# Performance work log

Measured on AMD Instinct MI355X. Metric: run time of the kernel, lower is better.

## Reference

```python
import jax, jax.numpy as jnp
import numpy as np


def dct_matrices(N):
    # torch_dct-style unnormalized DCT-II (norm=None): X_k = 2 * sum_n x_n cos(pi*(2n+1)k/(2N))
    n = jnp.arange(N, dtype=jnp.float32)
    ang = jnp.pi * (2.0 * n[None, :] + 1.0) * n[:, None] / (2.0 * N)  # [k, n]
    D = 2.0 * jnp.cos(ang)                                            # forward DCT matrix [k, n]
    w = jnp.where(n == 0, 0.5, 1.0)                                   # half-weight on DC term
    M = (jnp.cos(ang).T * w[None, :]) / (2.0 * N)                     # inverse DCT matrix [n, k]
    return D, M


def setup_inputs() -> dict:
    key = jax.random.key(0)
    k1, k2, k3 = jax.random.split(key, 3)
    B, c_in, c_out, H, W, kh, kw = 8, 64, 128, 128, 128, 5, 5
    K = float(np.sqrt(1.0 / (c_in * kh * kw)))
    x = jax.random.normal(k1, (B, c_in, H, W), dtype=jnp.float32)
    weight = (2.0 * jax.random.uniform(k2, (c_out, c_in, kh, kw), dtype=jnp.float32) - 1.0) * K
    bias = (2.0 * jax.random.uniform(k3, (c_out,), dtype=jnp.float32) - 1.0) * K
    return {"x": x, "weight": weight, "bias": bias}


def reference(x, weight, bias):
    B, c_in, H, W = x.shape
    c_out, _, kh, kw = weight.shape
    D, M = dct_matrices(H)

    # DCT-II along H axis of input
    xd = jnp.einsum('kh,bchw->bckw', D, x)            # (B, c_in, H, W)
    xf = jnp.fft.rfft(xd, axis=-1)                    # (B, c_in, H, Wf) complex

    # Pad kernel along H to full size, DCT along H, rFFT along W with n=W
    wpad = jnp.pad(weight, ((0, 0), (0, 0), (0, H - kh), (0, 0)))
    wd = jnp.einsum('kh,oihw->oikw', D, wpad)         # (c_out, c_in, H, kw)
    wf = jnp.fft.rfft(wd, n=W, axis=-1)               # (c_out, c_in, H, Wf) complex

    # Broadcast complex multiply + reduce over c_in (fused via einsum)
    hf = jnp.einsum('bchw,ochw->bohw', xf, wf)        # (B, c_out, H, Wf)
    h = jnp.fft.irfft(hf, n=W, axis=-1)               # (B, c_out, H, W)

    # Inverse DCT along H, add bias, stride slice (stride = 1)
    h = jnp.einsum('nk,bokw->bonw', M, h) + bias[None, :, None, None]
    return h[:, :, ::1, ::1]
```

## Files before the change

### kernel.cpp

```cpp
#include <hip/hip_runtime.h>


using half8v = __attribute__((ext_vector_type(8))) _Float16;
using half4v = __attribute__((ext_vector_type(4))) _Float16;
using f32x4  = __attribute__((ext_vector_type(4))) float;

#define PI_F 3.14159265358979323846f

__device__ __forceinline__ int sw_off(int n, int k, int K, int mask) {
    int c = k >> 3;
    return n * K + (((c ^ (n & mask)) << 3) | (k & 7));
}

__global__ void k_dm(_Float16* __restrict__ D, _Float16* __restrict__ M) {
    int k = blockIdx.x;
    int h = threadIdx.x;
    float ang = PI_F * (float)((2 * h + 1) * k) * (1.0f / 256.0f);
    float c = cosf(ang);
    D[k * 128 + h] = (_Float16)(2.0f * c);
    float wk = (k == 0) ? 0.5f : 1.0f;
    M[h * 128 + k] = (_Float16)(c * wk * (1.0f / 256.0f));
}

__global__ __launch_bounds__(256) void k_wd(const float* __restrict__ w, _Float16* __restrict__ WD) {
    __shared__ float lw[1600];
    __shared__ float lcos[320];
    int co = blockIdx.x >> 1, k0 = (blockIdx.x & 1) << 6;
    int tid = threadIdx.x;

    for (int e = tid; e < 1600; e += 256) lw[e] = w[co * 1600 + e];
    for (int e = tid; e < 320; e += 256) {
        int kl = e / 5, i = e - kl * 5;
        lcos[e] = 2.0f * cosf(PI_F * (float)((2 * i + 1) * (k0 + kl)) * (1.0f / 256.0f));
    }
    __syncthreads();

    for (int e = tid; e < 20480; e += 256) {
        int kk = e & 31, rest = e >> 5;
        int s = rest % 10, kl = rest / 10;
        int j = s >> 1, ci = ((s & 1) << 5) + kk;
        const float* wp = &lw[ci * 25 + j];
        const float* cp = &lcos[kl * 5];
        float acc = 0.f;
#pragma unroll
        for (int i = 0; i < 5; ++i) acc += cp[i] * wp[i * 5];
        WD[(((long)(k0 + kl) * 10 + s) * 128 + co) * 32 + kk] = (_Float16)acc;
    }
}

__device__ __forceinline__ void gemm128_gA(const _Float16* __restrict__ gA,
                                           const _Float16* lB,
                                           f32x4 acc[4][4], int tid) {
    int lane = tid & 63, ln = lane & 15, q = lane >> 4;
    int wave = tid >> 6, wm = wave >> 1, wn = wave & 1;
#pragma unroll
    for (int s = 0; s < 4; ++s) {
        half8v af[4], bf[4];
#pragma unroll
        for (int mt = 0; mt < 4; ++mt) {
            int m = wm * 64 + mt * 16 + ln;
            af[mt] = *(const half8v*)(&gA[m * 128 + (s * 4 + q) * 8]);
        }
#pragma unroll
        for (int nt = 0; nt < 4; ++nt) {
            int n = wn * 64 + nt * 16 + ln;
            bf[nt] = *(const half8v*)(&lB[n * 128 + (((s * 4 + q) ^ (n & 15)) << 3)]);
        }
#pragma unroll
        for (int mt = 0; mt < 4; ++mt)
#pragma unroll
            for (int nt = 0; nt < 4; ++nt)
                acc[mt][nt] = __builtin_amdgcn_mfma_f32_16x16x32_f16(af[mt], bf[nt], acc[mt][nt], 0, 0, 0);
    }
}

__device__ __forceinline__ void stage_transB(const _Float16* __restrict__ src, int row_stride,
                                             _Float16* l, int K, int mask, int nblocks, int tid) {
    for (int blk = tid; blk < nblocks; blk += 256) {
        int kb = blk >> 4, wb = blk & 15;
        int k0 = kb * 4, w0 = wb * 8;
        half8v r0 = *(const half8v*)(&src[(k0 + 0) * row_stride + w0]);
        half8v r1 = *(const half8v*)(&src[(k0 + 1) * row_stride + w0]);
        half8v r2 = *(const half8v*)(&src[(k0 + 2) * row_stride + w0]);
        half8v r3 = *(const half8v*)(&src[(k0 + 3) * row_stride + w0]);
#pragma unroll
        for (int dw = 0; dw < 8; ++dw) {
            int n = w0 + dw;
            half4v p = {r0[dw], r1[dw], r2[dw], r3[dw]};
            *(half4v*)(&l[sw_off(n, k0, K, mask)]) = p;
        }
    }
}

__global__ __launch_bounds__(256) void k_dctH(const float* __restrict__ x,
                                              const _Float16* __restrict__ Dg,
                                              _Float16* __restrict__ xd) {
    __shared__ _Float16 lB[128 * 128];
    int b = blockIdx.x >> 6, ci = blockIdx.x & 63;
    int tid = threadIdx.x;

    const float* xs = x + (long)(b * 64 + ci) * 16384;
#pragma unroll
    for (int rep = 0; rep < 2; ++rep) {
        int blk = tid + rep * 256;
        int hb = blk >> 4, wb = blk & 15;
        int h0 = hb * 4, w0 = wb * 8;
        f32x4 f[4][2];
#pragma unroll
        for (int dh = 0; dh < 4; ++dh) {
            f[dh][0] = *(const f32x4*)(&xs[(h0 + dh) * 128 + w0]);
            f[dh][1] = *(const f32x4*)(&xs[(h0 + dh) * 128 + w0 + 4]);
        }
#pragma unroll
        for (int dw = 0; dw < 8; ++dw) {
            int n = w0 + dw;
            half4v p = {(_Float16)f[0][dw >> 2][dw & 3], (_Float16)f[1][dw >> 2][dw & 3],
                        (_Float16)f[2][dw >> 2][dw & 3], (_Float16)f[3][dw >> 2][dw & 3]};
            *(half4v*)(&lB[sw_off(n, h0, 128, 15)]) = p;
        }
    }
    __syncthreads();

    f32x4 acc[4][4] = {};
    gemm128_gA(Dg, lB, acc, tid);

    int lane = tid & 63, ln = lane & 15, q = lane >> 4;
    int wave = tid >> 6, wm = wave >> 1, wn = wave & 1;
#pragma unroll
    for (int mt = 0; mt < 4; ++mt)
#pragma unroll
        for (int nt = 0; nt < 4; ++nt)
#pragma unroll
            for (int r = 0; r < 4; ++r) {
                int kk = wm * 64 + mt * 16 + q * 4 + r;
                int wcol = wn * 64 + nt * 16 + ln;
                xd[((long)(kk * 8 + b) * 64 + ci) * 128 + wcol] = (_Float16)acc[mt][nt][r];
            }
}

__global__ __launch_bounds__(256) void k_conv(const _Float16* __restrict__ xd,
                                              const _Float16* __restrict__ WD,
                                              _Float16* __restrict__ y2) {
    __shared__ _Float16 lX[128 * 64];
    int bid = blockIdx.x;
    int k = bid & 127, b = bid >> 7;
    int tid = threadIdx.x;

    const _Float16* xs = xd + (long)(k * 8 + b) * 8192;
    stage_transB(xs, 128, lX, 64, 7, 256, tid);
    __syncthreads();

    int lane = tid & 63, ln = lane & 15, q = lane >> 4;
    int wave = tid >> 6, wm = wave >> 1, wn = wave & 1;
    f32x4 acc[4][4] = {};

    const _Float16* wkb = WD + (long)k * 40960;

    for (int s = 0; s < 10; ++s) {
        int j = s >> 1;
        int cb = (s & 1) << 2;
        const _Float16* wt = wkb + s * 4096;
        half8v af[4], bf[4];
#pragma unroll
        for (int mt = 0; mt < 4; ++mt) {
            int m = wm * 64 + mt * 16 + ln;
            af[mt] = *(const half8v*)(&wt[m * 32 + q * 8]);
        }
#pragma unroll
        for (int nt = 0; nt < 4; ++nt) {
            int wcol = wn * 64 + nt * 16 + ln;
            int n = (wcol - j) & 127;
            bf[nt] = *(const half8v*)(&lX[n * 64 + (((cb + q) ^ (n & 7)) << 3)]);
        }
#pragma unroll
        for (int mt = 0; mt < 4; ++mt)
#pragma unroll
            for (int nt = 0; nt < 4; ++nt)
                acc[mt][nt] = __builtin_amdgcn_mfma_f32_16x16x32_f16(af[mt], bf[nt], acc[mt][nt], 0, 0, 0);
    }

    _Float16* yb = y2 + (long)(b * 128 + k) * 16384;
#pragma unroll
    for (int mt = 0; mt < 4; ++mt)
#pragma unroll
        for (int nt = 0; nt < 4; ++nt)
#pragma unroll
            for (int r = 0; r < 4; ++r) {
                int co = wm * 64 + mt * 16 + q * 4 + r;
                int wcol = wn * 64 + nt * 16 + ln;
                yb[co * 128 + wcol] = (_Float16)acc[mt][nt][r];
            }
}

__global__ __launch_bounds__(256) void k_idct(const _Float16* __restrict__ y2,
                                              const _Float16* __restrict__ Mg,
                                              const float* __restrict__ bias,
                                              float* __restrict__ out) {
    __shared__ _Float16 lB[128 * 128];
    int b = blockIdx.x >> 7, co = blockIdx.x & 127;
    int tid = threadIdx.x;

    const _Float16* src = y2 + (long)b * 2097152 + co * 128;
    stage_transB(src, 16384, lB, 128, 15, 512, tid);
    __syncthreads();

    f32x4 acc[4][4] = {};
    gemm128_gA(Mg, lB, acc, tid);

    float bv = bias[co];
    float* ob = out + ((long)(b * 128 + co)) * 16384;
    int lane = tid & 63, ln = lane & 15, q = lane >> 4;
    int wave = tid >> 6, wm = wave >> 1, wn = wave & 1;
#pragma unroll
    for (int mt = 0; mt < 4; ++mt)
#pragma unroll
        for (int nt = 0; nt < 4; ++nt)
#pragma unroll
            for (int r = 0; r < 4; ++r) {
                int h = wm * 64 + mt * 16 + q * 4 + r;
                int wcol = wn * 64 + nt * 16 + ln;
                ob[h * 128 + wcol] = acc[mt][nt][r] + bv;
            }
}

extern "C" void kernel_launch(void* const* d_in, const int* in_sizes, int n_in,
                              void* d_out, int out_size, void* d_ws, size_t ws_size,
                              hipStream_t stream) {
    const float* x    = (const float*)d_in[0];
    const float* w    = (const float*)d_in[1];
    const float* bias = (const float*)d_in[2];
    float* out = (float*)d_out;

    char* ws = (char*)d_ws;
    _Float16* D  = (_Float16*)(ws);
    _Float16* M  = (_Float16*)(ws + 32768);
    _Float16* WD = (_Float16*)(ws + 65536);
    _Float16* xd = (_Float16*)(ws + 65536 + 10485760);
    _Float16* y2 = (_Float16*)(ws + 65536 + 10485760 + 16777216);

    k_dm  <<<dim3(128),  dim3(128), 0, stream>>>(D, M);
    k_wd  <<<dim3(256),  dim3(256), 0, stream>>>(w, WD);
    k_dctH<<<dim3(512),  dim3(256), 0, stream>>>(x, D, xd);
    k_conv<<<dim3(1024), dim3(256), 0, stream>>>(xd, WD, y2);
    k_idct<<<dim3(1024), dim3(256), 0, stream>>>(y2, M, bias, out);
}
```

Measured before the change: 149.1 us.

## Double-buffer conv weights via async LDS loads, merge prep kernels, relayout y2

Result: faster. 144.6 us (-3.0%).

```diff
diff --git a/kernel.cpp b/kernel.cpp
--- a/kernel.cpp
+++ b/kernel.cpp
@@ -12,17 +12,15 @@
     return n * K + (((c ^ (n & mask)) << 3) | (k & 7));
 }
 
-__global__ void k_dm(_Float16* __restrict__ D, _Float16* __restrict__ M) {
-    int k = blockIdx.x;
-    int h = threadIdx.x;
-    float ang = PI_F * (float)((2 * h + 1) * k) * (1.0f / 256.0f);
-    float c = cosf(ang);
-    D[k * 128 + h] = (_Float16)(2.0f * c);
-    float wk = (k == 0) ? 0.5f : 1.0f;
-    M[h * 128 + k] = (_Float16)(c * wk * (1.0f / 256.0f));
-}
-
-__global__ __launch_bounds__(256) void k_wd(const float* __restrict__ w, _Float16* __restrict__ WD) {
+__device__ __forceinline__ void gload16(const _Float16* g, _Float16* l) {
+    __builtin_amdgcn_global_load_lds((const __attribute__((address_space(1))) void*)g,
+                                     (__attribute__((address_space(3))) void*)l, 16, 0, 0);
+}
+
+__global__ __launch_bounds__(256) void k_prep(const float* __restrict__ w,
+                                              _Float16* __restrict__ WD,
+                                              _Float16* __restrict__ D,
+                                              _Float16* __restrict__ M) {
     __shared__ float lw[1600];
     __shared__ float lcos[320];
     int co = blockIdx.x >> 1, k0 = (blockIdx.x & 1) << 6;
@@ -32,6 +30,15 @@
     for (int e = tid; e < 320; e += 256) {
         int kl = e / 5, i = e - kl * 5;
         lcos[e] = 2.0f * cosf(PI_F * (float)((2 * i + 1) * (k0 + kl)) * (1.0f / 256.0f));
+    }
+    if (tid < 64) {
+        int g = blockIdx.x * 64 + tid;
+        int k = g >> 7, h = g & 127;
+        float ang = PI_F * (float)((2 * h + 1) * k) * (1.0f / 256.0f);
+        float c = cosf(ang);
+        D[k * 128 + h] = (_Float16)(2.0f * c);
+        float wk = (k == 0) ? 0.5f : 1.0f;
+        M[h * 128 + k] = (_Float16)(c * wk * (1.0f / 256.0f));
     }
     __syncthreads();
 
@@ -142,24 +149,38 @@
                                               const _Float16* __restrict__ WD,
                                               _Float16* __restrict__ y2) {
     __shared__ _Float16 lX[128 * 64];
+    __shared__ _Float16 lW[2 * 4096];
     int bid = blockIdx.x;
     int k = bid & 127, b = bid >> 7;
     int tid = threadIdx.x;
+    int lane = tid & 63, wave = tid >> 6;
 
     const _Float16* xs = xd + (long)(k * 8 + b) * 8192;
     stage_transB(xs, 128, lX, 64, 7, 256, tid);
-    __syncthreads();
-
-    int lane = tid & 63, ln = lane & 15, q = lane >> 4;
-    int wave = tid >> 6, wm = wave >> 1, wn = wave & 1;
+
+    const _Float16* wkb = WD + (long)k * 40960;
+    {
+        int eo = wave * 512 + lane * 8;
+        gload16(&wkb[eo],            &lW[wave * 512]);
+        gload16(&wkb[2048 + eo],     &lW[2048 + wave * 512]);
+        gload16(&wkb[4096 + eo],     &lW[4096 + wave * 512]);
+        gload16(&wkb[6144 + eo],     &lW[4096 + 2048 + wave * 512]);
+    }
+    __syncthreads();
+
+    int ln = lane & 15, q = lane >> 4;
+    int wm = wave >> 1, wn = wave & 1;
     f32x4 acc[4][4] = {};
 
-    const _Float16* wkb = WD + (long)k * 40960;
-
     for (int s = 0; s < 10; ++s) {
+        if (s == 9) asm volatile("s_waitcnt vmcnt(0)" ::: "memory");
+        else        asm volatile("s_waitcnt vmcnt(2)" ::: "memory");
+        __builtin_amdgcn_s_barrier();
+        asm volatile("" ::: "memory");
+
+        const _Float16* wt = &lW[(s & 1) * 4096];
         int j = s >> 1;
         int cb = (s & 1) << 2;
-        const _Float16* wt = wkb + s * 4096;
         half8v af[4], bf[4];
 #pragma unroll
         for (int mt = 0; mt < 4; ++mt) {
@@ -172,14 +193,25 @@
             int n = (wcol - j) & 127;
             bf[nt] = *(const half8v*)(&lX[n * 64 + (((cb + q) ^ (n & 7)) << 3)]);
         }
+        __builtin_amdgcn_s_setprio(1);
 #pragma unroll
         for (int mt = 0; mt < 4; ++mt)
 #pragma unroll
             for (int nt = 0; nt < 4; ++nt)
                 acc[mt][nt] = __builtin_amdgcn_mfma_f32_16x16x32_f16(af[mt], bf[nt], acc[mt][nt], 0, 0, 0);
-    }
-
-    _Float16* yb = y2 + (long)(b * 128 + k) * 16384;
+        __builtin_amdgcn_s_setprio(0);
+
+        asm volatile("" ::: "memory");
+        __builtin_amdgcn_s_barrier();
+        if (s < 8) {
+            const _Float16* gs = wkb + (s + 2) * 4096;
+            int eo = wave * 512 + lane * 8;
+            gload16(&gs[eo],        &lW[(s & 1) * 4096 + wave * 512]);
+            gload16(&gs[2048 + eo], &lW[(s & 1) * 4096 + 2048 + wave * 512]);
+        }
+    }
+
+    _Float16* yb = y2 + (long)b * 2097152 + k * 128;
 #pragma unroll
     for (int mt = 0; mt < 4; ++mt)
 #pragma unroll
@@ -188,7 +220,7 @@
             for (int r = 0; r < 4; ++r) {
                 int co = wm * 64 + mt * 16 + q * 4 + r;
                 int wcol = wn * 64 + nt * 16 + ln;
-                yb[co * 128 + wcol] = (_Float16)acc[mt][nt][r];
+                yb[(long)co * 16384 + wcol] = (_Float16)acc[mt][nt][r];
             }
 }
 
@@ -200,8 +232,8 @@
     int b = blockIdx.x >> 7, co = blockIdx.x & 127;
     int tid = threadIdx.x;
 
-    const _Float16* src = y2 + (long)b * 2097152 + co * 128;
-    stage_transB(src, 16384, lB, 128, 15, 512, tid);
+    const _Float16* src = y2 + (long)b * 2097152 + (long)co * 16384;
+    stage_transB(src, 128, lB, 128, 15, 512, tid);
     __syncthreads();
 
     f32x4 acc[4][4] = {};
@@ -238,8 +270,7 @@
     _Float16* xd = (_Float16*)(ws + 65536 + 10485760);
     _Float16* y2 = (_Float16*)(ws + 65536 + 10485760 + 16777216);
 
-    k_dm  <<<dim3(128),  dim3(128), 0, stream>>>(D, M);
-    k_wd  <<<dim3(256),  dim3(256), 0, stream>>>(w, WD);
+    k_prep<<<dim3(256),  dim3(256), 0, stream>>>(w, WD, D, M);
     k_dctH<<<dim3(512),  dim3(256), 0, stream>>>(x, D, xd);
     k_conv<<<dim3(1024), dim3(256), 0, stream>>>(xd, WD, y2);
     k_idct<<<dim3(1024), dim3(256), 0, stream>>>(y2, M, bias, out);
```
